# Kernel optimization log

Measured on AMD Instinct MI355X. Metric: run time of the kernel, lower is better.

## Reference

```python
import jax, jax.numpy as jnp
import numpy as np

N_NODES = 300000
N_EDGES = 1200000
D = 128
B = 1000
VOCAB = 26  # vocab_size + 1


def setup_inputs() -> dict:
    key = jax.random.key(0)
    ks = jax.random.split(key, 10)
    x = jax.random.randint(ks[0], (N_NODES,), 0, VOCAB, dtype=jnp.int32)
    edge_index = jax.random.randint(ks[1], (2, N_EDGES), 0, N_NODES, dtype=jnp.int32)
    # cumulative protein boundaries: B proteins of equal length, last entry == N_NODES
    amino_acids_numbers = (jnp.arange(1, B + 1, dtype=jnp.int32) * (N_NODES // B))
    s = 1.0 / np.sqrt(D)
    emb = jax.random.normal(ks[2], (VOCAB, D), dtype=jnp.float32)
    W_rel1 = jax.random.uniform(ks[3], (D, D), jnp.float32, -s, s)
    b_rel1 = jax.random.uniform(ks[4], (D,), jnp.float32, -s, s)
    W_root1 = jax.random.uniform(ks[5], (D, D), jnp.float32, -s, s)
    W_rel2 = jax.random.uniform(ks[6], (D, D), jnp.float32, -s, s)
    b_rel2 = jax.random.uniform(ks[7], (D,), jnp.float32, -s, s)
    W_root2 = jax.random.uniform(ks[8], (D, D), jnp.float32, -s, s)
    return {"x": x, "edge_index": edge_index, "amino_acids_numbers": amino_acids_numbers,
            "emb": emb, "W_rel1": W_rel1, "b_rel1": b_rel1, "W_root1": W_root1,
            "W_rel2": W_rel2, "b_rel2": b_rel2, "W_root2": W_root2}


def _graph_conv(nodes, src, tgt, W_rel, b_rel, W_root, n):
    # PyG GraphConv (aggr='add'): out = Lin_rel(sum_{j->i} x_j) + Lin_root(x_i)
    agg = jax.ops.segment_sum(nodes[src], tgt, num_segments=n)  # [N, D]
    return agg @ W_rel.T + b_rel + nodes @ W_root.T


def reference(x, edge_index, amino_acids_numbers, emb,
              W_rel1, b_rel1, W_root1, W_rel2, b_rel2, W_root2):
    n = x.shape[0]
    src, tgt = edge_index[0], edge_index[1]
    nodes = emb[x]  # [N, D] embedding lookup
    nodes = _graph_conv(nodes, src, tgt, W_rel1, b_rel1, W_root1, n)
    nodes = _graph_conv(nodes, src, tgt, W_rel2, b_rel2, W_root2, n)
    # segment mean pooling over [start:end) slices defined by cumulative ends
    ends = amino_acids_numbers
    seg = jnp.searchsorted(ends, jnp.arange(n), side='right')  # node -> protein id
    b = ends.shape[0]
    sums = jax.ops.segment_sum(nodes, seg, num_segments=b)  # [B, D]
    counts = jnp.diff(ends, prepend=jnp.zeros((1,), ends.dtype)).astype(nodes.dtype)
    return sums / counts[:, None]
```

## Files before the change

### kernel.cpp

```cpp
#include <hip/hip_runtime.h>

#define DD 128
#define VV 26
#define NW 13
#define CS8 8
#define G 256
#define TWIN 512

__device__ __forceinline__ unsigned wsum(unsigned v) {
#pragma unroll
    for (int m = 32; m >= 1; m >>= 1) v += __shfl_xor(v, m, 64);
    return v;
}

__device__ __forceinline__ int wscan_incl(int v) {
    int lane = threadIdx.x & 63;
#pragma unroll
    for (int off = 1; off < 64; off <<= 1) {
        int t = __shfl_up(v, off, 64);
        if (lane >= off) v += t;
    }
    return v;
}

__device__ __forceinline__ int seg_guess(const int* ends, int B, int t, int Lavg) {
    int p = t / Lavg;
    if (p > B - 1) p = B - 1;
    while (p > 0 && ends[p - 1] > t) --p;
    while (ends[p] <= t) ++p;
    return p;
}

__device__ __forceinline__ int bseg(const int* cumx, int j) {
    int lo = 0, hi = G - 1;
    while (lo < hi) {
        int mid = (lo + hi + 1) >> 1;
        if (cumx[mid] <= j) lo = mid; else hi = mid - 1;
    }
    return lo;
}

__global__ __launch_bounds__(1024)
void k_sort_pre(const int* __restrict__ src, const int* __restrict__ tgt,
                const int* __restrict__ x, const int* __restrict__ ends,
                int E, int B, int chunk, int Lavg,
                const float* __restrict__ emb,
                const float* __restrict__ W1r, const float* __restrict__ b1,
                const float* __restrict__ W1o,
                const float* __restrict__ W2r, const float* __restrict__ W2o,
                unsigned short* __restrict__ sorted_tl, unsigned* __restrict__ sorted_s,
                int* __restrict__ segstart, int* __restrict__ seghist,
                float* __restrict__ P1, float* __restrict__ P2,
                float* __restrict__ P3, float* __restrict__ uvec,
                float* __restrict__ wvec) {
    extern __shared__ int lds[];
    int tid = threadIdx.x;
    int chunkp = (chunk + 1) & ~1;

    if (blockIdx.x >= G) {
        float* e1r = (float*)lds;
        float* r1r = e1r + DD;
        float* b1s = r1r + DD;
        int v = blockIdx.x - G;
        int d = tid;
        if (d < DD) {
            const float* e = emb + v * DD;
            const float* w1r = W1r + d * DD;
            const float* w1o = W1o + d * DD;
            float s1 = 0.f, s2 = 0.f;
            for (int k = 0; k < DD; ++k) { float ev = e[k]; s1 += ev * w1r[k]; s2 += ev * w1o[k]; }
            e1r[d] = s1; r1r[d] = s2; b1s[d] = b1[d];
        }
        __syncthreads();
        if (d < DD) {
            const float* wr = W2r + d * DD;
            const float* wo = W2o + d * DD;
            float p1 = 0.f, p2 = 0.f, p3 = 0.f, su = 0.f, sw = 0.f;
            for (int k = 0; k < DD; ++k) {
                float a = wr[k], bb = wo[k], ee = e1r[k], r = r1r[k], c = b1s[k];
                p1 += ee * a; p2 += r * a + ee * bb; p3 += r * bb;
                su += c * a; sw += c * bb;
            }
            P1[v * DD + d] = p1; P2[v * DD + d] = p2; P3[v * DD + d] = p3;
            if (v == 0) { uvec[d] = su; wvec[d] = sw; }
        }
        return;
    }

    int* lds_ends = lds;
    int* hist = lds_ends + 1024;
    int* cur = hist + 1024;
    int* wsums = cur + 1024;
    unsigned short* lpe = (unsigned short*)(wsums + 16);
    unsigned short* stl = lpe + chunkp;
    unsigned* sts = (unsigned*)(stl + chunkp);

    int b = blockIdx.x;
    int e0 = b * chunk;
    int e1 = min(E, e0 + chunk);
    int clen = e1 - e0;

    for (int i = tid; i < B; i += 1024) lds_ends[i] = ends[i];
    hist[tid] = 0;
    __syncthreads();

    for (int i = tid; i < clen; i += 1024) {
        int t = tgt[e0 + i];
        int p = seg_guess(lds_ends, B, t, Lavg);
        atomicAdd(&hist[p], 1);
        lpe[i] = (unsigned short)p;
    }
    __syncthreads();

    int v = hist[tid];
    if (tid < B) seghist[b * B + tid] = v;
    int wave = tid >> 6, lane = tid & 63;
    int incl = wscan_incl(v);
    if (lane == 63) wsums[wave] = incl;
    __syncthreads();
    int offw = 0;
    for (int w = 0; w < wave; ++w) offw += wsums[w];
    int excl = incl + offw - v;
    if (tid < B) {
        cur[tid] = excl;
        segstart[b * B + tid] = e0 + excl;
    }
    __syncthreads();

    for (int i = tid; i < clen; i += 1024) {
        int e = e0 + i;
        int p = lpe[i];
        int s = src[e];
        int t = tgt[e];
        int lbl = x[s];
        int pst = (p == 0) ? 0 : lds_ends[p - 1];
        int pos = atomicAdd(&cur[p], 1);
        stl[pos] = (unsigned short)(((t - pst) << 5) | lbl);
        sts[pos] = (unsigned)s;
    }
    __syncthreads();

    for (int i = tid; i < clen; i += 1024) {
        sorted_tl[e0 + i] = stl[i];
        sorted_s[e0 + i] = sts[i];
    }
}

__global__ __launch_bounds__(256)
void k_trans(const int* __restrict__ a, const int* __restrict__ c, int B,
             int* __restrict__ aT, int* __restrict__ cT) {
    __shared__ int ta[32][33], tc[32][33];
    int b0 = blockIdx.x * 32;
    int p0 = blockIdx.y * 32;
    int tx = threadIdx.x & 31, ty = threadIdx.x >> 5;
    for (int r = ty; r < 32; r += 8) {
        int bb = b0 + r, pp = p0 + tx;
        if (pp < B) { ta[r][tx] = a[bb * B + pp]; tc[r][tx] = c[bb * B + pp]; }
    }
    __syncthreads();
    for (int r = ty; r < 32; r += 8) {
        int pp = p0 + r, bb = b0 + tx;
        if (pp < B) { aT[pp * G + bb] = ta[tx][r]; cT[pp * G + bb] = tc[tx][r]; }
    }
}

__global__ __launch_bounds__(256)
void k_counts(const int* __restrict__ x, const int* __restrict__ ends,
              const int* __restrict__ seghistT, const int* __restrict__ segstartT,
              int B, int E, const unsigned short* __restrict__ sorted_tl,
              unsigned* __restrict__ counts,
              float* __restrict__ CpG, float* __restrict__ HpG) {
    __shared__ unsigned tab[TWIN * CS8];
    __shared__ int cumx[G + 4], segb[G], wsums[4];
    __shared__ unsigned red[4][2 * NW];
    int p = blockIdx.x, tid = threadIdx.x;
    int wave = tid >> 6, lane = tid & 63;
    int start = (p == 0) ? 0 : ends[p - 1];
    int end = ends[p];
    int Lp = end - start;

    int h = seghistT[p * G + tid];
    segb[tid] = segstartT[p * G + tid];
    int incl = wscan_incl(h);
    if (lane == 63) wsums[wave] = incl;
    __syncthreads();
    int offw = 0;
    for (int w = 0; w < wave; ++w) offw += wsums[w];
    cumx[tid] = incl + offw - h;
    if (tid == 255) cumx[G] = incl + offw;
    __syncthreads();
    int Dp = cumx[G];

    unsigned cpw[NW], hpw[NW];
#pragma unroll
    for (int w = 0; w < NW; ++w) { cpw[w] = 0u; hpw[w] = 0u; }

    for (int i = start + tid; i < end; i += 256) {
        int l = x[i];
        unsigned inc = 1u << ((l & 1) * 16);
        int wi = l >> 1;
#pragma unroll
        for (int w = 0; w < NW; ++w) hpw[w] += (w == wi) ? inc : 0u;
    }

    for (int w0 = 0; w0 < Lp; w0 += TWIN) {
        int wlen = min(TWIN, Lp - w0);
        __syncthreads();
        for (int i = tid; i < wlen * CS8; i += 256) tab[i] = 0u;
        __syncthreads();
        for (int j = tid; j < Dp; j += 256) {
            int bb = bseg(cumx, j);
            int pos = segb[bb] + (j - cumx[bb]);
            unsigned tl = (unsigned)sorted_tl[pos];
            int lbl = (int)(tl & 31u);
            int tloc = (int)(tl >> 5) - w0;
            if ((unsigned)tloc < (unsigned)wlen)
                atomicAdd(&tab[tloc * CS8 + (lbl >> 2)], 1u << ((lbl & 3) * 8));
            if (w0 == 0) {
                unsigned inc = 1u << ((lbl & 1) * 16);
                int wi = lbl >> 1;
#pragma unroll
                for (int w = 0; w < NW; ++w) cpw[w] += (w == wi) ? inc : 0u;
            }
        }
        __syncthreads();
        for (int idx = tid; idx < wlen * CS8; idx += 256) {
            int r = idx >> 3, w = idx & 7;
            counts[((size_t)(start + w0 + r)) * CS8 + w] = tab[r * CS8 + w];
        }
    }

#pragma unroll
    for (int w = 0; w < NW; ++w) {
        unsigned a = wsum(cpw[w]); if (lane == 0) red[wave][w] = a;
        unsigned b = wsum(hpw[w]); if (lane == 0) red[wave][NW + w] = b;
    }
    __syncthreads();
    if (tid < 2 * NW) {
        unsigned t = red[0][tid] + red[1][tid] + red[2][tid] + red[3][tid];
        int grp = tid / NW, w = tid % NW;
        float* dst = (grp == 0) ? (CpG + (size_t)p * VV) : (HpG + (size_t)p * VV);
        dst[w * 2] = (float)(t & 0xFFFFu);
        if (w * 2 + 1 < VV) dst[w * 2 + 1] = (float)(t >> 16);
    }
}

__global__ __launch_bounds__(256)
void k_protein(const int* __restrict__ ends,
               const int* __restrict__ seghistT, const int* __restrict__ segstartT,
               const unsigned* __restrict__ sorted_s,
               const unsigned* __restrict__ counts,
               const float* __restrict__ CpG, const float* __restrict__ HpG,
               const float* __restrict__ P1, const float* __restrict__ P2,
               const float* __restrict__ P3, const float* __restrict__ uvec,
               const float* __restrict__ wvec, const float* __restrict__ b2,
               int B, int E, float* __restrict__ out) {
    __shared__ int cumx[G + 4], segb[G], wsums[4];
    __shared__ unsigned red[4][14];
    __shared__ float c2f[VV], cpf[VV], hpf[VV];
    int p = blockIdx.x, tid = threadIdx.x;
    int wave = tid >> 6, lane = tid & 63;
    int start = (p == 0) ? 0 : ends[p - 1];
    int end = ends[p];

    int h = seghistT[p * G + tid];
    segb[tid] = segstartT[p * G + tid];
    int incl = wscan_incl(h);
    if (lane == 63) wsums[wave] = incl;
    __syncthreads();
    int offw = 0;
    for (int w = 0; w < wave; ++w) offw += wsums[w];
    cumx[tid] = incl + offw - h;
    if (tid == 255) cumx[G] = incl + offw;
    __syncthreads();
    int Dp = cumx[G];

    unsigned ua[7], ub[7];
#pragma unroll
    for (int k = 0; k < 7; ++k) { ua[k] = 0u; ub[k] = 0u; }
    for (int j = tid; j < Dp; j += 256) {
        int bb = bseg(cumx, j);
        int pos = segb[bb] + (j - cumx[bb]);
        int s = (int)sorted_s[pos];
        const uint4* cb = reinterpret_cast<const uint4*>(counts + (size_t)s * CS8);
        uint4 c0 = cb[0], c1 = cb[1];
        unsigned w;
        w = c0.x; ua[0] += w & 0x00FF00FFu; ub[0] += (w >> 8) & 0x00FF00FFu;
        w = c0.y; ua[1] += w & 0x00FF00FFu; ub[1] += (w >> 8) & 0x00FF00FFu;
        w = c0.z; ua[2] += w & 0x00FF00FFu; ub[2] += (w >> 8) & 0x00FF00FFu;
        w = c0.w; ua[3] += w & 0x00FF00FFu; ub[3] += (w >> 8) & 0x00FF00FFu;
        w = c1.x; ua[4] += w & 0x00FF00FFu; ub[4] += (w >> 8) & 0x00FF00FFu;
        w = c1.y; ua[5] += w & 0x00FF00FFu; ub[5] += (w >> 8) & 0x00FF00FFu;
        w = c1.z; ua[6] += w & 0x00FF00FFu; ub[6] += (w >> 8) & 0x00FF00FFu;
    }

#pragma unroll
    for (int k = 0; k < 7; ++k) {
        unsigned a = wsum(ua[k]); if (lane == 0) red[wave][2 * k] = a;
        unsigned b = wsum(ub[k]); if (lane == 0) red[wave][2 * k + 1] = b;
    }
    if (tid >= 64 && tid < 64 + VV)   cpf[tid - 64]  = CpG[(size_t)p * VV + (tid - 64)];
    if (tid >= 128 && tid < 128 + VV) hpf[tid - 128] = HpG[(size_t)p * VV + (tid - 128)];
    __syncthreads();
    if (tid < 14) {
        unsigned t = red[0][tid] + red[1][tid] + red[2][tid] + red[3][tid];
        int k = tid >> 1, isB = tid & 1;
        int base = 4 * k + isB;
        c2f[base] = (float)(t & 0xFFFFu);
        if (base + 2 < VV) c2f[base + 2] = (float)(t >> 16);
    }
    __syncthreads();

    if (tid < DD) {
        int d = tid;
        float acc = 0.f;
#pragma unroll
        for (int v = 0; v < VV; ++v)
            acc += c2f[v] * P1[v * DD + d] + cpf[v] * P2[v * DD + d] + hpf[v] * P3[v * DD + d];
        float Lp = (float)(end - start);
        float invL = 1.f / Lp;
        float Dpf = (float)Dp;
        out[(size_t)p * DD + d] = acc * invL + (Dpf * invL) * uvec[d] + wvec[d] + b2[d];
    }
}

extern "C" void kernel_launch(void* const* d_in, const int* in_sizes, int n_in,
                              void* d_out, int out_size, void* d_ws, size_t ws_size,
                              hipStream_t stream) {
    const int*   x       = (const int*)d_in[0];
    const int*   edge    = (const int*)d_in[1];
    const int*   ends    = (const int*)d_in[2];
    const float* emb     = (const float*)d_in[3];
    const float* W_rel1  = (const float*)d_in[4];
    const float* b_rel1  = (const float*)d_in[5];
    const float* W_root1 = (const float*)d_in[6];
    const float* W_rel2  = (const float*)d_in[7];
    const float* b_rel2  = (const float*)d_in[8];
    const float* W_root2 = (const float*)d_in[9];

    const int N = in_sizes[0];
    const int E = in_sizes[1] / 2;
    const int B = in_sizes[2];
    const int Lavg = (N / B) > 0 ? (N / B) : 1;
    const int chunk = (E + G - 1) / G;
    const int chunkp = (chunk + 1) & ~1;

    const int* srcp = edge;
    const int* tgtp = edge + E;

    auto align256 = [](size_t v) { return (v + 255) & ~(size_t)255; };
    char* ws = (char*)d_ws;
    size_t off = 0;
    unsigned* counts = (unsigned*)(ws + off);                off += align256((size_t)N * CS8 * 4);
    int* segstart = (int*)(ws + off);                        off += align256((size_t)G * B * 4);
    int* seghist = (int*)(ws + off);                         off += align256((size_t)G * B * 4);
    int* segstartT = (int*)(ws + off);                       off += align256((size_t)B * G * 4);
    int* seghistT = (int*)(ws + off);                        off += align256((size_t)B * G * 4);
    unsigned short* sorted_tl = (unsigned short*)(ws + off); off += align256((size_t)E * 2);
    unsigned* sorted_s = (unsigned*)(ws + off);              off += align256((size_t)E * 4);
    float* CpG = (float*)(ws + off);                         off += align256((size_t)B * VV * 4);
    float* HpG = (float*)(ws + off);                         off += align256((size_t)B * VV * 4);
    float* P1 = (float*)(ws + off);                          off += align256((size_t)VV * DD * 4);
    float* P2 = (float*)(ws + off);                          off += align256((size_t)VV * DD * 4);
    float* P3 = (float*)(ws + off);                          off += align256((size_t)VV * DD * 4);
    float* uvec = (float*)(ws + off);                        off += align256((size_t)DD * 4);
    float* wvec = (float*)(ws + off);                        off += align256((size_t)DD * 4);
    (void)ws_size; (void)n_in; (void)out_size;


    size_t ldsb = (size_t)(3 * 1024 + 16) * 4 + (size_t)chunkp * 4 + (size_t)chunk * 4;
    k_sort_pre<<<G + VV, 1024, ldsb, stream>>>(
        srcp, tgtp, x, ends, E, B, chunk, Lavg,
        emb, W_rel1, b_rel1, W_root1, W_rel2, W_root2,
        sorted_tl, sorted_s, segstart, seghist, P1, P2, P3, uvec, wvec);

    dim3 tgrid(G / 32, (B + 31) / 32);
    k_trans<<<tgrid, 256, 0, stream>>>(seghist, segstart, B, seghistT, segstartT);

    k_counts<<<B, 256, 0, stream>>>(x, ends, seghistT, segstartT, B, E, sorted_tl,
                                    counts, CpG, HpG);

    k_protein<<<B, 256, 0, stream>>>(ends, seghistT, segstartT, sorted_s, counts, CpG, HpG,
                                     P1, P2, P3, uvec, wvec, b_rel2, B, E, (float*)d_out);
}
```

Measured before the change: 70.93 us.

## Write transposed segment tables directly and move label histograms into protein kernel

The sort kernel now writes its per-chunk segment histogram and start tables straight into transposed layout, so the separate transpose kernel and one launch go away. The per-protein label histograms (CpG/HpG) are no longer built in k_counts. k_protein derives the in-edge label counts by summing the per-node count rows, which removes the register-heavy 13-word accumulation from k_counts. The trade-off is that the transposed global writes are strided, and k_protein does extra passes over counts and x.

```diff
diff --git a/kernel.cpp b/kernel.cpp
--- a/kernel.cpp
+++ b/kernel.cpp
@@ -49,7 +49,7 @@
                 const float* __restrict__ W1o,
                 const float* __restrict__ W2r, const float* __restrict__ W2o,
                 unsigned short* __restrict__ sorted_tl, unsigned* __restrict__ sorted_s,
-                int* __restrict__ segstart, int* __restrict__ seghist,
+                int* __restrict__ segstartT, int* __restrict__ seghistT,
                 float* __restrict__ P1, float* __restrict__ P2,
                 float* __restrict__ P3, float* __restrict__ uvec,
                 float* __restrict__ wvec) {
@@ -113,7 +113,7 @@
     __syncthreads();
 
     int v = hist[tid];
-    if (tid < B) seghist[b * B + tid] = v;
+    if (tid < B) seghistT[tid * G + b] = v;
     int wave = tid >> 6, lane = tid & 63;
     int incl = wscan_incl(v);
     if (lane == 63) wsums[wave] = incl;
@@ -123,7 +123,7 @@
     int excl = incl + offw - v;
     if (tid < B) {
         cur[tid] = excl;
-        segstart[b * B + tid] = e0 + excl;
+        segstartT[tid * G + b] = e0 + excl;
     }
     __syncthreads();
 
@@ -147,32 +147,12 @@
 }
 
 __global__ __launch_bounds__(256)
-void k_trans(const int* __restrict__ a, const int* __restrict__ c, int B,
-             int* __restrict__ aT, int* __restrict__ cT) {
-    __shared__ int ta[32][33], tc[32][33];
-    int b0 = blockIdx.x * 32;
-    int p0 = blockIdx.y * 32;
-    int tx = threadIdx.x & 31, ty = threadIdx.x >> 5;
-    for (int r = ty; r < 32; r += 8) {
-        int bb = b0 + r, pp = p0 + tx;
-        if (pp < B) { ta[r][tx] = a[bb * B + pp]; tc[r][tx] = c[bb * B + pp]; }
-    }
-    __syncthreads();
-    for (int r = ty; r < 32; r += 8) {
-        int pp = p0 + r, bb = b0 + tx;
-        if (pp < B) { aT[pp * G + bb] = ta[tx][r]; cT[pp * G + bb] = tc[tx][r]; }
-    }
-}
-
-__global__ __launch_bounds__(256)
-void k_counts(const int* __restrict__ x, const int* __restrict__ ends,
+void k_counts(const int* __restrict__ ends,
               const int* __restrict__ seghistT, const int* __restrict__ segstartT,
               int B, int E, const unsigned short* __restrict__ sorted_tl,
-              unsigned* __restrict__ counts,
-              float* __restrict__ CpG, float* __restrict__ HpG) {
+              unsigned* __restrict__ counts) {
     __shared__ unsigned tab[TWIN * CS8];
     __shared__ int cumx[G + 4], segb[G], wsums[4];
-    __shared__ unsigned red[4][2 * NW];
     int p = blockIdx.x, tid = threadIdx.x;
     int wave = tid >> 6, lane = tid & 63;
     int start = (p == 0) ? 0 : ends[p - 1];
@@ -190,18 +170,6 @@
     if (tid == 255) cumx[G] = incl + offw;
     __syncthreads();
     int Dp = cumx[G];
-
-    unsigned cpw[NW], hpw[NW];
-#pragma unroll
-    for (int w = 0; w < NW; ++w) { cpw[w] = 0u; hpw[w] = 0u; }
-
-    for (int i = start + tid; i < end; i += 256) {
-        int l = x[i];
-        unsigned inc = 1u << ((l & 1) * 16);
-        int wi = l >> 1;
-#pragma unroll
-        for (int w = 0; w < NW; ++w) hpw[w] += (w == wi) ? inc : 0u;
-    }
 
     for (int w0 = 0; w0 < Lp; w0 += TWIN) {
         int wlen = min(TWIN, Lp - w0);
@@ -216,12 +184,6 @@
             int tloc = (int)(tl >> 5) - w0;
             if ((unsigned)tloc < (unsigned)wlen)
                 atomicAdd(&tab[tloc * CS8 + (lbl >> 2)], 1u << ((lbl & 3) * 8));
-            if (w0 == 0) {
-                unsigned inc = 1u << ((lbl & 1) * 16);
-                int wi = lbl >> 1;
-#pragma unroll
-                for (int w = 0; w < NW; ++w) cpw[w] += (w == wi) ? inc : 0u;
-            }
         }
         __syncthreads();
         for (int idx = tid; idx < wlen * CS8; idx += 256) {
@@ -229,34 +191,19 @@
             counts[((size_t)(start + w0 + r)) * CS8 + w] = tab[r * CS8 + w];
         }
     }
-
-#pragma unroll
-    for (int w = 0; w < NW; ++w) {
-        unsigned a = wsum(cpw[w]); if (lane == 0) red[wave][w] = a;
-        unsigned b = wsum(hpw[w]); if (lane == 0) red[wave][NW + w] = b;
-    }
-    __syncthreads();
-    if (tid < 2 * NW) {
-        unsigned t = red[0][tid] + red[1][tid] + red[2][tid] + red[3][tid];
-        int grp = tid / NW, w = tid % NW;
-        float* dst = (grp == 0) ? (CpG + (size_t)p * VV) : (HpG + (size_t)p * VV);
-        dst[w * 2] = (float)(t & 0xFFFFu);
-        if (w * 2 + 1 < VV) dst[w * 2 + 1] = (float)(t >> 16);
-    }
 }
 
 __global__ __launch_bounds__(256)
-void k_protein(const int* __restrict__ ends,
+void k_protein(const int* __restrict__ x, const int* __restrict__ ends,
                const int* __restrict__ seghistT, const int* __restrict__ segstartT,
                const unsigned* __restrict__ sorted_s,
                const unsigned* __restrict__ counts,
-               const float* __restrict__ CpG, const float* __restrict__ HpG,
                const float* __restrict__ P1, const float* __restrict__ P2,
                const float* __restrict__ P3, const float* __restrict__ uvec,
                const float* __restrict__ wvec, const float* __restrict__ b2,
                int B, int E, float* __restrict__ out) {
     __shared__ int cumx[G + 4], segb[G], wsums[4];
-    __shared__ unsigned red[4][14];
+    __shared__ unsigned red[4][48];
     __shared__ float c2f[VV], cpf[VV], hpf[VV];
     int p = blockIdx.x, tid = threadIdx.x;
     int wave = tid >> 6, lane = tid & 63;
@@ -275,9 +222,12 @@
     __syncthreads();
     int Dp = cumx[G];
 
-    unsigned ua[7], ub[7];
-#pragma unroll
-    for (int k = 0; k < 7; ++k) { ua[k] = 0u; ub[k] = 0u; }
+    unsigned c2a[7], c2b[7], cpa[7], cpb[7], hpw[NW];
+#pragma unroll
+    for (int k = 0; k < 7; ++k) { c2a[k] = 0u; c2b[k] = 0u; cpa[k] = 0u; cpb[k] = 0u; }
+#pragma unroll
+    for (int w = 0; w < NW; ++w) hpw[w] = 0u;
+
     for (int j = tid; j < Dp; j += 256) {
         int bb = bseg(cumx, j);
         int pos = segb[bb] + (j - cumx[bb]);
@@ -285,29 +235,67 @@
         const uint4* cb = reinterpret_cast<const uint4*>(counts + (size_t)s * CS8);
         uint4 c0 = cb[0], c1 = cb[1];
         unsigned w;
-        w = c0.x; ua[0] += w & 0x00FF00FFu; ub[0] += (w >> 8) & 0x00FF00FFu;
-        w = c0.y; ua[1] += w & 0x00FF00FFu; ub[1] += (w >> 8) & 0x00FF00FFu;
-        w = c0.z; ua[2] += w & 0x00FF00FFu; ub[2] += (w >> 8) & 0x00FF00FFu;
-        w = c0.w; ua[3] += w & 0x00FF00FFu; ub[3] += (w >> 8) & 0x00FF00FFu;
-        w = c1.x; ua[4] += w & 0x00FF00FFu; ub[4] += (w >> 8) & 0x00FF00FFu;
-        w = c1.y; ua[5] += w & 0x00FF00FFu; ub[5] += (w >> 8) & 0x00FF00FFu;
-        w = c1.z; ua[6] += w & 0x00FF00FFu; ub[6] += (w >> 8) & 0x00FF00FFu;
+        w = c0.x; c2a[0] += w & 0x00FF00FFu; c2b[0] += (w >> 8) & 0x00FF00FFu;
+        w = c0.y; c2a[1] += w & 0x00FF00FFu; c2b[1] += (w >> 8) & 0x00FF00FFu;
+        w = c0.z; c2a[2] += w & 0x00FF00FFu; c2b[2] += (w >> 8) & 0x00FF00FFu;
+        w = c0.w; c2a[3] += w & 0x00FF00FFu; c2b[3] += (w >> 8) & 0x00FF00FFu;
+        w = c1.x; c2a[4] += w & 0x00FF00FFu; c2b[4] += (w >> 8) & 0x00FF00FFu;
+        w = c1.y; c2a[5] += w & 0x00FF00FFu; c2b[5] += (w >> 8) & 0x00FF00FFu;
+        w = c1.z; c2a[6] += w & 0x00FF00FFu; c2b[6] += (w >> 8) & 0x00FF00FFu;
+    }
+
+    for (int i = start + tid; i < end; i += 256) {
+        const uint4* cb = reinterpret_cast<const uint4*>(counts + (size_t)i * CS8);
+        uint4 c0 = cb[0], c1 = cb[1];
+        unsigned w;
+        w = c0.x; cpa[0] += w & 0x00FF00FFu; cpb[0] += (w >> 8) & 0x00FF00FFu;
+        w = c0.y; cpa[1] += w & 0x00FF00FFu; cpb[1] += (w >> 8) & 0x00FF00FFu;
+        w = c0.z; cpa[2] += w & 0x00FF00FFu; cpb[2] += (w >> 8) & 0x00FF00FFu;
+        w = c0.w; cpa[3] += w & 0x00FF00FFu; cpb[3] += (w >> 8) & 0x00FF00FFu;
+        w = c1.x; cpa[4] += w & 0x00FF00FFu; cpb[4] += (w >> 8) & 0x00FF00FFu;
+        w = c1.y; cpa[5] += w & 0x00FF00FFu; cpb[5] += (w >> 8) & 0x00FF00FFu;
+        w = c1.z; cpa[6] += w & 0x00FF00FFu; cpb[6] += (w >> 8) & 0x00FF00FFu;
+    }
+
+    for (int i = start + tid; i < end; i += 256) {
+        int l = x[i];
+        unsigned inc = 1u << ((l & 1) * 16);
+        int wi = l >> 1;
+#pragma unroll
+        for (int w = 0; w < NW; ++w) hpw[w] += (w == wi) ? inc : 0u;
     }
 
 #pragma unroll
     for (int k = 0; k < 7; ++k) {
-        unsigned a = wsum(ua[k]); if (lane == 0) red[wave][2 * k] = a;
-        unsigned b = wsum(ub[k]); if (lane == 0) red[wave][2 * k + 1] = b;
-    }
-    if (tid >= 64 && tid < 64 + VV)   cpf[tid - 64]  = CpG[(size_t)p * VV + (tid - 64)];
-    if (tid >= 128 && tid < 128 + VV) hpf[tid - 128] = HpG[(size_t)p * VV + (tid - 128)];
-    __syncthreads();
-    if (tid < 14) {
+        unsigned a, b;
+        a = wsum(c2a[k]); if (lane == 0) red[wave][2 * k] = a;
+        b = wsum(c2b[k]); if (lane == 0) red[wave][2 * k + 1] = b;
+        a = wsum(cpa[k]); if (lane == 0) red[wave][16 + 2 * k] = a;
+        b = wsum(cpb[k]); if (lane == 0) red[wave][16 + 2 * k + 1] = b;
+    }
+#pragma unroll
+    for (int w = 0; w < NW; ++w) {
+        unsigned a = wsum(hpw[w]); if (lane == 0) red[wave][32 + w] = a;
+    }
+    __syncthreads();
+    if (tid < 48) {
         unsigned t = red[0][tid] + red[1][tid] + red[2][tid] + red[3][tid];
-        int k = tid >> 1, isB = tid & 1;
-        int base = 4 * k + isB;
-        c2f[base] = (float)(t & 0xFFFFu);
-        if (base + 2 < VV) c2f[base + 2] = (float)(t >> 16);
+        if (tid < 14) {
+            int k = tid >> 1, isB = tid & 1;
+            int base = 4 * k + isB;
+            c2f[base] = (float)(t & 0xFFFFu);
+            if (base + 2 < VV) c2f[base + 2] = (float)(t >> 16);
+        } else if (tid >= 16 && tid < 30) {
+            int q = tid - 16;
+            int k = q >> 1, isB = q & 1;
+            int base = 4 * k + isB;
+            cpf[base] = (float)(t & 0xFFFFu);
+            if (base + 2 < VV) cpf[base + 2] = (float)(t >> 16);
+        } else if (tid >= 32 && tid < 32 + NW) {
+            int w = tid - 32;
+            hpf[w * 2] = (float)(t & 0xFFFFu);
+            if (w * 2 + 1 < VV) hpf[w * 2 + 1] = (float)(t >> 16);
+        }
     }
     __syncthreads();
 
@@ -352,14 +340,10 @@
     char* ws = (char*)d_ws;
     size_t off = 0;
     unsigned* counts = (unsigned*)(ws + off);                off += align256((size_t)N * CS8 * 4);
-    int* segstart = (int*)(ws + off);                        off += align256((size_t)G * B * 4);
-    int* seghist = (int*)(ws + off);                         off += align256((size_t)G * B * 4);
     int* segstartT = (int*)(ws + off);                       off += align256((size_t)B * G * 4);
     int* seghistT = (int*)(ws + off);                        off += align256((size_t)B * G * 4);
     unsigned short* sorted_tl = (unsigned short*)(ws + off); off += align256((size_t)E * 2);
     unsigned* sorted_s = (unsigned*)(ws + off);              off += align256((size_t)E * 4);
-    float* CpG = (float*)(ws + off);                         off += align256((size_t)B * VV * 4);
-    float* HpG = (float*)(ws + off);                         off += align256((size_t)B * VV * 4);
     float* P1 = (float*)(ws + off);                          off += align256((size_t)VV * DD * 4);
     float* P2 = (float*)(ws + off);                          off += align256((size_t)VV * DD * 4);
     float* P3 = (float*)(ws + off);                          off += align256((size_t)VV * DD * 4);
@@ -372,14 +356,10 @@
     k_sort_pre<<<G + VV, 1024, ldsb, stream>>>(
         srcp, tgtp, x, ends, E, B, chunk, Lavg,
         emb, W_rel1, b_rel1, W_root1, W_rel2, W_root2,
-        sorted_tl, sorted_s, segstart, seghist, P1, P2, P3, uvec, wvec);
-
-    dim3 tgrid(G / 32, (B + 31) / 32);
-    k_trans<<<tgrid, 256, 0, stream>>>(seghist, segstart, B, seghistT, segstartT);
-
-    k_counts<<<B, 256, 0, stream>>>(x, ends, seghistT, segstartT, B, E, sorted_tl,
-                                    counts, CpG, HpG);
-
-    k_protein<<<B, 256, 0, stream>>>(ends, seghistT, segstartT, sorted_s, counts, CpG, HpG,
+        sorted_tl, sorted_s, segstartT, seghistT, P1, P2, P3, uvec, wvec);
+
+    k_counts<<<B, 256, 0, stream>>>(ends, seghistT, segstartT, B, E, sorted_tl, counts);
+
+    k_protein<<<B, 256, 0, stream>>>(x, ends, seghistT, segstartT, sorted_s, counts,
                                      P1, P2, P3, uvec, wvec, b_rel2, B, E, (float*)d_out);
 }
```

After: 71.78 us. Within noise of the previous version (+1.2%).
